# Kernel optimization log

Hardware: AMD Instinct MI355X
Metric: run time of the kernel (lower is better)

Reference implementation:

```python
import jax, jax.numpy as jnp
import numpy as np
from jax import lax

D_MODEL = 128
D_INNER = 256   # expand * d_model
D_STATE = 16
D_CONV = 4
DT_RANK = 8     # ceil(d_model / 16)
IN_CH = 64
SCALE = 0.02


def setup_inputs() -> dict:
    key = jax.random.key(0)
    ks = jax.random.split(key, 16)
    r = lambda k, s: jax.random.normal(k, s, dtype=jnp.float32)
    return {
        "x": r(ks[0], (4, IN_CH, 128, 128)),
        "conv_w": r(ks[1], (D_MODEL, IN_CH, 3, 3)) * SCALE,
        "conv_b": r(ks[2], (D_MODEL,)) * SCALE,
        "bn_g": jnp.ones((D_MODEL,), jnp.float32),
        "bn_b": jnp.zeros((D_MODEL,), jnp.float32),
        "bn_mean": r(ks[3], (D_MODEL,)) * SCALE,
        "bn_var": jax.random.uniform(ks[4], (D_MODEL,), jnp.float32) + 0.5,
        "in_w": r(ks[5], (2 * D_INNER, D_MODEL)) * SCALE,
        "conv1d_w": r(ks[6], (D_INNER, 1, D_CONV)) * SCALE,
        "conv1d_b": r(ks[7], (D_INNER,)) * SCALE,
        "xproj_w": r(ks[8], (DT_RANK + 2 * D_STATE, D_INNER)) * SCALE,
        "dtproj_w": r(ks[9], (D_INNER, DT_RANK)) * SCALE,
        "dtproj_b": r(ks[10], (D_INNER,)) * SCALE,
        "A_log": r(ks[11], (D_INNER, D_STATE)) * 0.5,
        "Dp": r(ks[12], (D_INNER,)) * SCALE,
        "out_w": r(ks[13], (D_MODEL, D_INNER)) * SCALE,
    }


def _mamba(u, in_w, conv1d_w, conv1d_b, xproj_w, dtproj_w, dtproj_b, A_log, Dp, out_w):
    # u: [B, L, d_model]
    xz = jnp.einsum("bld,ed->ble", u, in_w)          # [B, L, 2*d_inner]
    x_in, z = jnp.split(xz, 2, axis=-1)
    # depthwise causal conv1d over L
    xc = lax.conv_general_dilated(
        x_in.transpose(0, 2, 1), conv1d_w, (1,), [(D_CONV - 1, 0)],
        dimension_numbers=("NCL", "OIL", "NCL"), feature_group_count=D_INNER,
    ) + conv1d_b[None, :, None]
    x_in = jax.nn.silu(xc).transpose(0, 2, 1)         # [B, L, d_inner]

    x_dbl = jnp.einsum("bld,ed->ble", x_in, xproj_w)  # [B, L, dt_rank+2*d_state]
    dt, Bm, Cm = jnp.split(x_dbl, [DT_RANK, DT_RANK + D_STATE], axis=-1)
    delta = jax.nn.softplus(jnp.einsum("blr,dr->bld", dt, dtproj_w) + dtproj_b)

    A = -jnp.exp(A_log)                               # [d_inner, d_state]
    deltaA = jnp.exp(jnp.einsum("bld,dn->bldn", delta, A))        # [B,L,d,n]
    deltaBu = jnp.einsum("bld,bln,bld->bldn", delta, Bm, x_in)    # [B,L,d,n]

    def step(h, inp):
        dA, dBu, c = inp                              # [B,d,n],[B,d,n],[B,n]
        h = dA * h + dBu
        y = jnp.einsum("bdn,bn->bd", h, c)
        return h, y

    Bsz, L = u.shape[0], u.shape[1]
    h0 = jnp.zeros((Bsz, D_INNER, D_STATE), u.dtype)
    _, ys = lax.scan(step, h0, (deltaA.transpose(1, 0, 2, 3),
                                deltaBu.transpose(1, 0, 2, 3),
                                Cm.transpose(1, 0, 2)))
    y = ys.transpose(1, 0, 2) + x_in * Dp             # [B, L, d_inner]
    y = y * jax.nn.silu(z)
    return jnp.einsum("bld,ed->ble", y, out_w)        # [B, L, d_model]


def reference(x, conv_w, conv_b, bn_g, bn_b, bn_mean, bn_var, in_w, conv1d_w,
              conv1d_b, xproj_w, dtproj_w, dtproj_b, A_log, Dp, out_w):
    # downsample: conv3x3 stride2 + BN(eval) + exact GELU
    y = lax.conv_general_dilated(x, conv_w, (2, 2), [(1, 1), (1, 1)],
                                 dimension_numbers=("NCHW", "OIHW", "NCHW"))
    y = y + conv_b[None, :, None, None]
    inv = bn_g / jnp.sqrt(bn_var + 1e-5)
    y = (y - bn_mean[None, :, None, None]) * inv[None, :, None, None] + bn_b[None, :, None, None]
    y = jax.nn.gelu(y, approximate=False)             # [B, C, H, W]

    B, C, H, W = y.shape
    u = y.reshape(B, C, H * W).transpose(0, 2, 1)     # [B, L, C]
    out = _mamba(u, in_w, conv1d_w, conv1d_b, xproj_w, dtproj_w, dtproj_b,
                 A_log, Dp, out_w)
    out = out.transpose(0, 2, 1).reshape(B, C, H, W)
    return y + out
```

## Files before the change

### kernel.cpp

```cpp
#include <hip/hip_runtime.h>
#include <math.h>

#define NB 4
#define LTOK 4096
#define DM 128
#define DI 256
#define NCH 256
#define TCH 16
#define GSZ 16
#define NG  16

#define OFF_A2     0u
#define OFF_BIAS2  73728u
#define OFF_YDS    84096u
#define OFF_XPRE   2181248u
#define OFF_Z      6375552u
#define OFF_DELTA  10569856u
#define OFF_YABF   12667008u
#define OFF_BC     14764160u
#define OFF_DSUM   15288448u
#define OFF_GS     15550592u
#define OFF_GD     15812736u
#define OFF_XT     15829120u
#define OFF_WBF    17926272u
#define OFF_WCMP   17963136u
#define OFF_YDSBF  18004096u
#define OFF_INWBF  19052672u
#define OFF_OUTWBF 19085440u

#define DEV __device__ __forceinline__
#define L2E 1.4426950408889634f

typedef short bh8 __attribute__((ext_vector_type(8)));
typedef float f4v __attribute__((ext_vector_type(4)));

DEV float fast_silu(float v) {
  return v * __builtin_amdgcn_rcpf(1.f + __expf(-v));
}

DEV unsigned short f2bf(float f) {
  unsigned int u = __float_as_uint(f);
  u = (u + 0x7FFFu + ((u >> 16) & 1u)) >> 16;
  return (unsigned short)u;
}

DEV float bf2f(unsigned short us) {
  return __uint_as_float((unsigned int)us << 16);
}

__global__ __launch_bounds__(256) void k0_prep(
    const float* __restrict__ conv_w, const float* __restrict__ conv_b,
    const float* __restrict__ bn_g, const float* __restrict__ bn_b,
    const float* __restrict__ bn_mean, const float* __restrict__ bn_var,
    const float* __restrict__ xproj_w, const float* __restrict__ A_log,
    const float* __restrict__ dtw, const float* __restrict__ in_w,
    const float* __restrict__ out_w, float* __restrict__ ws) {
  int i = blockIdx.x * 256 + threadIdx.x;
  if (i < 73728) {
    int ci = i & 63; int tap = (i >> 6) % 9; int co = i / 576;
    float inv = bn_g[co] * rsqrtf(bn_var[co] + 1e-5f);
    ((unsigned short*)(ws + OFF_WBF))[i] = f2bf(conv_w[co * 576 + ci * 9 + tap] * inv);
  } else if (i < 73856) {
    int co = i - 73728;
    float inv = bn_g[co] * rsqrtf(bn_var[co] + 1e-5f);
    ws[OFF_BIAS2 + co] = (conv_b[co] - bn_mean[co]) * inv + bn_b[co];
  } else if (i < 77952) {
    int j = i - 73856;
    ws[OFF_A2 + j] = -__expf(A_log[j]) * L2E;
  } else if (i < 159872) {
    int j = i - 77952;
    int n = j >> 8, k = j & 255;
    float v = 0.f;
    if (n < 256) {
#pragma unroll
      for (int r = 0; r < 8; ++r)
        v = fmaf(dtw[n * 8 + r], xproj_w[r * 256 + k], v);
    } else if (n < 288) {
      v = xproj_w[(8 + n - 256) * 256 + k];
    }
    ((unsigned short*)(ws + OFF_WCMP))[j] = f2bf(v);
  } else if (i < 225408) {
    int j = i - 159872;
    ((unsigned short*)(ws + OFF_INWBF))[j] = f2bf(in_w[j]);
  } else if (i < 258176) {
    int j = i - 225408;
    ((unsigned short*)(ws + OFF_OUTWBF))[j] = f2bf(out_w[j]);
  }
}

__global__ __launch_bounds__(256) void k0b_transpose(
    const float* __restrict__ x, unsigned short* __restrict__ xt) {
  __shared__ float t[64][65];
  const int tid = threadIdx.x;
  const int ixh = blockIdx.x & 1;
  const int iy = (blockIdx.x >> 1) & 127;
  const int b = blockIdx.x >> 8;
  {
    const int ixl = tid & 63, cw = tid >> 6;
#pragma unroll 4
    for (int i = 0; i < 16; ++i) {
      int ci = cw * 16 + i;
      t[ci][ixl] = x[(((size_t)(b * 64 + ci) * 128) + iy) * 128 + ixh * 64 + ixl];
    }
  }
  __syncthreads();
  {
    const int cil = tid & 63, iw = tid >> 6;
    unsigned short* dst = xt + (((size_t)(b * 128 + iy) * 128) + ixh * 64) * 64;
#pragma unroll 4
    for (int i = 0; i < 16; ++i) {
      int ix = iw * 16 + i;
      dst[ix * 64 + cil] = f2bf(t[cil][ix]);
    }
  }
}

__global__ __launch_bounds__(256) void k1_conv_mfma(
    const unsigned short* __restrict__ xt, const unsigned short* __restrict__ wbf,
    const float* __restrict__ bias2, float* __restrict__ yds,
    unsigned short* __restrict__ ydsbf) {
  __shared__ unsigned short ldt[64][66];
  const int tid = threadIdx.x;
  const int lane = tid & 63;
  const int w = tid >> 6;
  const int col = lane & 15, quad = lane >> 4;
  const int cohalf = blockIdx.x & 1;
  const int oy = (blockIdx.x >> 1) & 63;
  const int b = blockIdx.x >> 7;
  const int co0 = cohalf * 64 + (w & 1) * 32;
  const int tok0 = (w >> 1) * 32;
  const int iy0 = 2 * oy - 1;
  const bh8 bzero = {};
  f4v acc[2][2];
#pragma unroll
  for (int mt = 0; mt < 2; ++mt)
#pragma unroll
    for (int nt = 0; nt < 2; ++nt) acc[mt][nt] = (f4v){0.f, 0.f, 0.f, 0.f};

  const unsigned short* ap0 = wbf + (size_t)(co0 + col) * 576;
  const unsigned short* ap1 = wbf + (size_t)(co0 + 16 + col) * 576;

  for (int tap = 0; tap < 9; ++tap) {
    const int kh = tap / 3, kw = tap - kh * 3;
    const int iy = iy0 + kh;
    const int ix0 = 2 * (tok0 + col) - 1 + kw;
    const int ix1 = ix0 + 32;
    const unsigned short* xrow = xt + (long)(b * 128 + iy) * 8192;
    const bool ok0 = (iy >= 0) && (ix0 >= 0);
    const bool ok1 = (iy >= 0);
#pragma unroll
    for (int kc = 0; kc < 2; ++kc) {
      const int cib = kc * 32 + quad * 8;
      bh8 a0 = *(const bh8*)&ap0[tap * 64 + cib];
      bh8 a1 = *(const bh8*)&ap1[tap * 64 + cib];
      bh8 b0 = *(const bh8*)&xrow[(long)ix0 * 64 + cib];
      bh8 b1 = *(const bh8*)&xrow[(long)ix1 * 64 + cib];
      if (!ok0) b0 = bzero;
      if (!ok1) b1 = bzero;
      acc[0][0] = __builtin_amdgcn_mfma_f32_16x16x32_bf16(a0, b0, acc[0][0], 0, 0, 0);
      acc[1][0] = __builtin_amdgcn_mfma_f32_16x16x32_bf16(a1, b0, acc[1][0], 0, 0, 0);
      acc[0][1] = __builtin_amdgcn_mfma_f32_16x16x32_bf16(a0, b1, acc[0][1], 0, 0, 0);
      acc[1][1] = __builtin_amdgcn_mfma_f32_16x16x32_bf16(a1, b1, acc[1][1], 0, 0, 0);
    }
  }
#pragma unroll
  for (int mt = 0; mt < 2; ++mt)
#pragma unroll
    for (int nt = 0; nt < 2; ++nt) {
      const int tok = tok0 + nt * 16 + col;
#pragma unroll
      for (int r = 0; r < 4; ++r) {
        const int co = co0 + mt * 16 + quad * 4 + r;
        float v = acc[mt][nt][r] + bias2[co];
        float g = 0.5f * v * (1.f + erff(v * 0.70710678118f));
        yds[(((size_t)(b * 128 + co) * 64) + oy) * 64 + tok] = g;
        ldt[tok][(w & 1) * 32 + mt * 16 + quad * 4 + r] = f2bf(g);
      }
    }
  __syncthreads();
  {
    const int tok = tid >> 2, cg = (tid & 3) * 16;
    unsigned short* dst =
        ydsbf + ((size_t)(b * 4096 + oy * 64 + tok)) * 128 + cohalf * 64 + cg;
#pragma unroll
    for (int j = 0; j < 8; ++j)
      ((unsigned int*)dst)[j] = *(const unsigned int*)&ldt[tok][cg + 2 * j];
  }
}

__global__ __launch_bounds__(256) void k2_mfma(
    const unsigned short* __restrict__ ydsbf, const unsigned short* __restrict__ inwbf,
    float* __restrict__ xpre, float* __restrict__ z) {
  const int tid = threadIdx.x;
  const int lane = tid & 63;
  const int w = tid >> 6;
  const int col = lane & 15, quad = lane >> 4;
  const int tt = blockIdx.x & 255, b = blockIdx.x >> 8;
  const int t0 = tt * 16;
  bh8 afrag[4];
  {
    const unsigned short* arow = ydsbf + (size_t)(b * 4096 + t0 + col) * 128 + quad * 8;
#pragma unroll
    for (int kb = 0; kb < 4; ++kb) afrag[kb] = *(const bh8*)&arow[kb * 32];
  }
  f4v acc[8];
#pragma unroll
  for (int j = 0; j < 8; ++j) acc[j] = (f4v){0.f, 0.f, 0.f, 0.f};
  const int nt0 = w * 8;
  const unsigned short* wb = inwbf + (size_t)(nt0 * 16 + col) * 128 + quad * 8;
#pragma unroll
  for (int kb = 0; kb < 4; ++kb) {
#pragma unroll
    for (int j = 0; j < 8; ++j) {
      bh8 bfrag = *(const bh8*)&wb[(size_t)j * 2048 + kb * 32];
      acc[j] = __builtin_amdgcn_mfma_f32_16x16x32_bf16(afrag[kb], bfrag, acc[j], 0, 0, 0);
    }
  }
#pragma unroll
  for (int j = 0; j < 8; ++j) {
    const int e = (nt0 + j) * 16 + col;
#pragma unroll
    for (int r = 0; r < 4; ++r) {
      const int t = t0 + quad * 4 + r;
      if (e < 256) xpre[((size_t)(b * 4096 + t)) * 256 + e] = acc[j][r];
      else z[((size_t)(b * 4096 + t)) * 256 + e - 256] = acc[j][r];
    }
  }
}

__global__ __launch_bounds__(256) void k3_conv1d_silu(
    const float* __restrict__ xpre, const float* __restrict__ w,
    const float* __restrict__ bvec, unsigned short* __restrict__ xinbf) {
  int i = blockIdx.x * 256 + threadIdx.x;
  int e4 = (i & 63) * 4;
  int t = (i >> 6) & 4095;
  int b = i >> 18;
  const float* base = xpre + (size_t)b * 4096 * 256;
  float4 zero = make_float4(0.f, 0.f, 0.f, 0.f);
  float4 r0 = (t >= 3) ? *(const float4*)&base[(size_t)(t - 3) * 256 + e4] : zero;
  float4 r1 = (t >= 2) ? *(const float4*)&base[(size_t)(t - 2) * 256 + e4] : zero;
  float4 r2 = (t >= 1) ? *(const float4*)&base[(size_t)(t - 1) * 256 + e4] : zero;
  float4 r3 = *(const float4*)&base[(size_t)t * 256 + e4];
  float4 w0 = *(const float4*)&w[(e4 + 0) * 4];
  float4 w1 = *(const float4*)&w[(e4 + 1) * 4];
  float4 w2 = *(const float4*)&w[(e4 + 2) * 4];
  float4 w3 = *(const float4*)&w[(e4 + 3) * 4];
  float4 bv = *(const float4*)&bvec[e4];
  float o0 = bv.x + w0.x * r0.x + w0.y * r1.x + w0.z * r2.x + w0.w * r3.x;
  float o1 = bv.y + w1.x * r0.y + w1.y * r1.y + w1.z * r2.y + w1.w * r3.y;
  float o2 = bv.z + w2.x * r0.z + w2.y * r1.z + w2.z * r2.z + w2.w * r3.z;
  float o3 = bv.w + w3.x * r0.w + w3.y * r1.w + w3.z * r2.w + w3.w * r3.w;
  float s0 = fast_silu(o0), s1 = fast_silu(o1), s2 = fast_silu(o2), s3 = fast_silu(o3);
  size_t off = ((size_t)b * 4096 + t) * 256 + e4;
  unsigned long long p = (unsigned long long)f2bf(s0)
                       | ((unsigned long long)f2bf(s1) << 16)
                       | ((unsigned long long)f2bf(s2) << 32)
                       | ((unsigned long long)f2bf(s3) << 48);
  *(unsigned long long*)&xinbf[off] = p;
}

__global__ __launch_bounds__(256) void k4_mfma(
    const unsigned short* __restrict__ wcomp, const float* __restrict__ dtb,
    const unsigned short* __restrict__ xinbf, unsigned short* __restrict__ delta,
    float* __restrict__ bc, float* __restrict__ dsum) {
  __shared__ unsigned short ld_delta[16][264];
  __shared__ float ld_bc[16][33];
  const int tid = threadIdx.x;
  const int lane = tid & 63;
  const int w = tid >> 6;
  const int col = lane & 15, quad = lane >> 4;
  const int tt = blockIdx.x & 255, b = blockIdx.x >> 8;
  const int t0 = tt * 16;

  bh8 afrag[8];
  {
    const unsigned short* arow = xinbf + (size_t)(b * 4096 + t0 + col) * 256 + quad * 8;
#pragma unroll
    for (int kb = 0; kb < 8; ++kb) afrag[kb] = *(const bh8*)&arow[kb * 32];
  }
  f4v acc[5];
#pragma unroll
  for (int j = 0; j < 5; ++j) acc[j] = (f4v){0.f, 0.f, 0.f, 0.f};

  const int nt0 = w * 5;
  const unsigned short* wb = wcomp + (size_t)(nt0 * 16 + col) * 256 + quad * 8;
#pragma unroll
  for (int kb = 0; kb < 8; ++kb) {
#pragma unroll
    for (int j = 0; j < 5; ++j) {
      bh8 bfrag = *(const bh8*)&wb[(size_t)j * 4096 + kb * 32];
      acc[j] = __builtin_amdgcn_mfma_f32_16x16x32_bf16(afrag[kb], bfrag, acc[j], 0, 0, 0);
    }
  }
#pragma unroll
  for (int j = 0; j < 5; ++j) {
    const int n = (nt0 + j) * 16 + col;
    if (n < 256) {
      float bias = dtb[n];
#pragma unroll
      for (int r = 0; r < 4; ++r) {
        float s = acc[j][r] + bias;
        float dl = fmaxf(s, 0.f) + __logf(1.f + __expf(-fabsf(s)));
        ld_delta[quad * 4 + r][n] = f2bf(dl);
      }
    } else if (n < 288) {
#pragma unroll
      for (int r = 0; r < 4; ++r) ld_bc[quad * 4 + r][n - 256] = acc[j][r];
    }
  }
  __syncthreads();

  {
    float ds = 0.f;
#pragma unroll
    for (int i = 0; i < 16; ++i) ds += bf2f(ld_delta[i][tid]);
    dsum[((size_t)b * 256 + tt) * 256 + tid] = ds;
  }
#pragma unroll
  for (int it = 0; it < 4; ++it) {
    int idx = it * 256 + tid;
    int row = idx >> 6, d4 = (idx & 63) * 4;
    unsigned long long pk = *(const unsigned long long*)&ld_delta[row][d4];
    *(unsigned long long*)&delta[((size_t)(b * 4096 + t0 + row)) * 256 + d4] = pk;
  }
  if (tid < 128) {
    int row = tid >> 3, q = (tid & 7) * 4;
    float4 v = make_float4(ld_bc[row][q], ld_bc[row][q + 1],
                           ld_bc[row][q + 2], ld_bc[row][q + 3]);
    *(float4*)&bc[((size_t)(b * 4096 + t0 + row)) * 32 + q] = v;
  }
}

__global__ __launch_bounds__(256) void k5a_scan1(
    const unsigned short* __restrict__ xinbf, const float* __restrict__ bc,
    const unsigned short* __restrict__ delta, const float* __restrict__ a2tab,
    float* __restrict__ S) {
  __shared__ __align__(16) float bct[TCH * 32];
  const int tid = threadIdx.x;
  const int d = tid;
  const int c = blockIdx.x & (NCH - 1), b = blockIdx.x >> 8;
  const int t0 = c * TCH;
  {
    const float* src = bc + (size_t)(b * 4096 + t0) * 32;
    for (int i = tid; i < TCH * 32; i += 256) bct[i] = src[i];
  }
  float A2[16];
#pragma unroll
  for (int j = 0; j < 4; ++j) {
    float4 a = *(const float4*)&a2tab[d * 16 + j * 4];
    A2[4 * j + 0] = a.x; A2[4 * j + 1] = a.y; A2[4 * j + 2] = a.z; A2[4 * j + 3] = a.w;
  }
  float h[16];
#pragma unroll
  for (int n = 0; n < 16; ++n) h[n] = 0.f;
  const unsigned short* pd = delta + (size_t)(b * 4096 + t0) * 256 + d;
  const unsigned short* px = xinbf + (size_t)(b * 4096 + t0) * 256 + d;
  __syncthreads();
#pragma unroll 4
  for (int i = 0; i < TCH; ++i) {
    float dl = bf2f(pd[(size_t)i * 256]);
    float xv = bf2f(px[(size_t)i * 256]);
    float dlx = dl * xv;
    const float* r = &bct[i * 32];
    float4 B0 = *(const float4*)&r[0];
    float4 B1 = *(const float4*)&r[4];
    float4 B2 = *(const float4*)&r[8];
    float4 B3 = *(const float4*)&r[12];
    float Bv[16] = {B0.x, B0.y, B0.z, B0.w, B1.x, B1.y, B1.z, B1.w,
                    B2.x, B2.y, B2.z, B2.w, B3.x, B3.y, B3.z, B3.w};
#pragma unroll
    for (int n = 0; n < 16; ++n)
      h[n] = fmaf(exp2f(dl * A2[n]), h[n], dlx * Bv[n]);
  }
  const size_t sbase = ((size_t)(b * NCH + c) * 16) * 256 + d;
#pragma unroll
  for (int n = 0; n < 16; ++n) S[sbase + (size_t)n * 256] = h[n];
}

__global__ __launch_bounds__(256) void k5b1_group(
    float* __restrict__ S, const float* __restrict__ dsum,
    const float* __restrict__ a2tab, float* __restrict__ Gs,
    float* __restrict__ Gd) {
  const int d = threadIdx.x;
  const int n = blockIdx.x & 15, g = (blockIdx.x >> 4) & (NG - 1),
            b = blockIdx.x >> 8;
  const float A2 = a2tab[d * 16 + n];
  float h = 0.f, cum = 0.f;
#pragma unroll 4
  for (int c16 = 0; c16 < GSZ; ++c16) {
    int c = g * GSZ + c16;
    size_t si = ((size_t)(b * NCH + c) * 16 + n) * 256 + d;
    float s = S[si];
    float dsv = dsum[((size_t)b * NCH + c) * 256 + d];
    float P = exp2f(A2 * dsv);
    S[si] = h;
    h = fmaf(P, h, s);
    cum += dsv;
  }
  Gs[((size_t)(b * NG + g) * 16 + n) * 256 + d] = h;
  if (n == 0) Gd[((size_t)b * NG + g) * 256 + d] = cum;
}

__global__ __launch_bounds__(256) void k5b2_groupscan(
    float* __restrict__ Gs, const float* __restrict__ Gd,
    const float* __restrict__ a2tab) {
  const int d = threadIdx.x;
  const int n = blockIdx.x & 15, b = blockIdx.x >> 4;
  const float A2 = a2tab[d * 16 + n];
  float h = 0.f;
#pragma unroll
  for (int g = 0; g < NG; ++g) {
    size_t gi = ((size_t)(b * NG + g) * 16 + n) * 256 + d;
    float s = Gs[gi];
    float P = exp2f(A2 * Gd[((size_t)b * NG + g) * 256 + d]);
    Gs[gi] = h;
    h = fmaf(P, h, s);
  }
}

__global__ __launch_bounds__(256) void k5c_scan2(
    const unsigned short* __restrict__ xinbf, const float* __restrict__ bc,
    const unsigned short* __restrict__ delta, const float* __restrict__ z,
    const float* __restrict__ a2tab, const float* __restrict__ Dp,
    const float* __restrict__ dsum, const float* __restrict__ Gs,
    const float* __restrict__ S, unsigned short* __restrict__ yabf) {
  __shared__ __align__(16) float bct[TCH * 32];
  const int tid = threadIdx.x;
  const int d = tid;
  const int c = blockIdx.x & (NCH - 1), b = blockIdx.x >> 8;
  const int t0 = c * TCH;
  {
    const float* src = bc + (size_t)(b * 4096 + t0) * 32;
    for (int i = tid; i < TCH * 32; i += 256) bct[i] = src[i];
  }
  float A2[16];
#pragma unroll
  for (int j = 0; j < 4; ++j) {
    float4 a = *(const float4*)&a2tab[d * 16 + j * 4];
    A2[4 * j + 0] = a.x; A2[4 * j + 1] = a.y; A2[4 * j + 2] = a.z; A2[4 * j + 3] = a.w;
  }
  const float Dpd = Dp[d];
  const int g = c >> 4, c16 = c & 15;
  float dpref = 0.f;
  {
    const float* pds = dsum + ((size_t)b * NCH + g * GSZ) * 256 + d;
    for (int cc = 0; cc < c16; ++cc) dpref += pds[(size_t)cc * 256];
  }
  const size_t sbase = ((size_t)(b * NCH + c) * 16) * 256 + d;
  const size_t gbase = ((size_t)(b * NG + g) * 16) * 256 + d;
  float h[16];
#pragma unroll
  for (int n = 0; n < 16; ++n) {
    float gi = Gs[gbase + (size_t)n * 256];
    float hl = S[sbase + (size_t)n * 256];
    h[n] = fmaf(exp2f(A2[n] * dpref), gi, hl);
  }
  const size_t base = (size_t)(b * 4096 + t0) * 256 + d;
  const unsigned short* pd = delta + base;
  const unsigned short* px = xinbf + base;
  const float* pz = z + base;
  unsigned short* py = yabf + base;
  __syncthreads();
#pragma unroll 4
  for (int i = 0; i < TCH; ++i) {
    float dl = bf2f(pd[(size_t)i * 256]);
    float xv = bf2f(px[(size_t)i * 256]);
    float zv = pz[(size_t)i * 256];
    float dlx = dl * xv;
    const float* r = &bct[i * 32];
    float4 B0 = *(const float4*)&r[0];
    float4 B1 = *(const float4*)&r[4];
    float4 B2 = *(const float4*)&r[8];
    float4 B3 = *(const float4*)&r[12];
    float4 C0 = *(const float4*)&r[16];
    float4 C1 = *(const float4*)&r[20];
    float4 C2 = *(const float4*)&r[24];
    float4 C3 = *(const float4*)&r[28];
    float Bv[16] = {B0.x, B0.y, B0.z, B0.w, B1.x, B1.y, B1.z, B1.w,
                    B2.x, B2.y, B2.z, B2.w, B3.x, B3.y, B3.z, B3.w};
    float Cv[16] = {C0.x, C0.y, C0.z, C0.w, C1.x, C1.y, C1.z, C1.w,
                    C2.x, C2.y, C2.z, C2.w, C3.x, C3.y, C3.z, C3.w};
    float y = 0.f;
#pragma unroll
    for (int n = 0; n < 16; ++n) {
      h[n] = fmaf(exp2f(dl * A2[n]), h[n], dlx * Bv[n]);
      y = fmaf(h[n], Cv[n], y);
    }
    py[(size_t)i * 256] = f2bf((y + xv * Dpd) * fast_silu(zv));
  }
}

__global__ __launch_bounds__(256) void k6_mfma(
    const unsigned short* __restrict__ yabf, const unsigned short* __restrict__ outwbf,
    const float* __restrict__ yds, float* __restrict__ out) {
  __shared__ float ld[16][132];
  const int tid = threadIdx.x;
  const int lane = tid & 63;
  const int w = tid >> 6;
  const int col = lane & 15, quad = lane >> 4;
  const int tt = blockIdx.x & 255, b = blockIdx.x >> 8;
  const int t0 = tt * 16;
  const int oy = t0 >> 6, ox0 = t0 & 63;
  bh8 afrag[8];
  {
    const unsigned short* arow = yabf + (size_t)(b * 4096 + t0 + col) * 256 + quad * 8;
#pragma unroll
    for (int kb = 0; kb < 8; ++kb) afrag[kb] = *(const bh8*)&arow[kb * 32];
  }
  f4v acc[2];
#pragma unroll
  for (int j = 0; j < 2; ++j) acc[j] = (f4v){0.f, 0.f, 0.f, 0.f};
  const int nt0 = w * 2;
  const unsigned short* wb = outwbf + (size_t)(nt0 * 16 + col) * 256 + quad * 8;
#pragma unroll
  for (int kb = 0; kb < 8; ++kb) {
#pragma unroll
    for (int j = 0; j < 2; ++j) {
      bh8 bfrag = *(const bh8*)&wb[(size_t)j * 4096 + kb * 32];
      acc[j] = __builtin_amdgcn_mfma_f32_16x16x32_bf16(afrag[kb], bfrag, acc[j], 0, 0, 0);
    }
  }
#pragma unroll
  for (int j = 0; j < 2; ++j)
#pragma unroll
    for (int r = 0; r < 4; ++r)
      ld[quad * 4 + r][(nt0 + j) * 16 + col] = acc[j][r];
  __syncthreads();
  {
    const int cc = tid >> 1, half = tid & 1;
    size_t base = (((size_t)(b * 128 + cc) * 64) + oy) * 64 + ox0 + half * 8;
    float4 r0 = *(const float4*)&yds[base];
    float4 r1 = *(const float4*)&yds[base + 4];
    const int m0 = half * 8;
    float4 o0 = make_float4(ld[m0 + 0][cc] + r0.x, ld[m0 + 1][cc] + r0.y,
                            ld[m0 + 2][cc] + r0.z, ld[m0 + 3][cc] + r0.w);
    float4 o1 = make_float4(ld[m0 + 4][cc] + r1.x, ld[m0 + 5][cc] + r1.y,
                            ld[m0 + 6][cc] + r1.z, ld[m0 + 7][cc] + r1.w);
    *(float4*)&out[base] = o0;
    *(float4*)&out[base + 4] = o1;
  }
}

extern "C" void kernel_launch(void* const* d_in, const int* in_sizes, int n_in,
                              void* d_out, int out_size, void* d_ws, size_t ws_size,
                              hipStream_t stream) {
  (void)in_sizes; (void)n_in; (void)out_size; (void)ws_size;
  const float* x        = (const float*)d_in[0];
  const float* conv_w   = (const float*)d_in[1];
  const float* conv_b   = (const float*)d_in[2];
  const float* bn_g     = (const float*)d_in[3];
  const float* bn_b     = (const float*)d_in[4];
  const float* bn_mean  = (const float*)d_in[5];
  const float* bn_var   = (const float*)d_in[6];
  const float* in_w     = (const float*)d_in[7];
  const float* conv1d_w = (const float*)d_in[8];
  const float* conv1d_b = (const float*)d_in[9];
  const float* xproj_w  = (const float*)d_in[10];
  const float* dtproj_w = (const float*)d_in[11];
  const float* dtproj_b = (const float*)d_in[12];
  const float* A_log    = (const float*)d_in[13];
  const float* Dp       = (const float*)d_in[14];
  const float* out_w    = (const float*)d_in[15];
  float* ws = (float*)d_ws;
  float* out = (float*)d_out;

  k0_prep<<<1009, 256, 0, stream>>>(conv_w, conv_b, bn_g, bn_b, bn_mean, bn_var,
                                    xproj_w, A_log, dtproj_w, in_w, out_w, ws);
  k0b_transpose<<<1024, 256, 0, stream>>>(x, (unsigned short*)(ws + OFF_XT));
  k1_conv_mfma<<<512, 256, 0, stream>>>((const unsigned short*)(ws + OFF_XT),
                                        (const unsigned short*)(ws + OFF_WBF),
                                        ws + OFF_BIAS2, ws + OFF_YDS,
                                        (unsigned short*)(ws + OFF_YDSBF));
  k2_mfma<<<1024, 256, 0, stream>>>((const unsigned short*)(ws + OFF_YDSBF),
                                    (const unsigned short*)(ws + OFF_INWBF),
                                    ws + OFF_XPRE, ws + OFF_Z);
  k3_conv1d_silu<<<4096, 256, 0, stream>>>(ws + OFF_XPRE, conv1d_w, conv1d_b,
                                           (unsigned short*)(ws + OFF_XT));
  k4_mfma<<<1024, 256, 0, stream>>>((const unsigned short*)(ws + OFF_WCMP),
                                    dtproj_b, (const unsigned short*)(ws + OFF_XT),
                                    (unsigned short*)(ws + OFF_DELTA),
                                    ws + OFF_BC, ws + OFF_DSUM);
  k5a_scan1<<<1024, 256, 0, stream>>>((const unsigned short*)(ws + OFF_XT),
                                      ws + OFF_BC,
                                      (const unsigned short*)(ws + OFF_DELTA),
                                      ws + OFF_A2, ws + OFF_XPRE);
  k5b1_group<<<1024, 256, 0, stream>>>(ws + OFF_XPRE, ws + OFF_DSUM, ws + OFF_A2,
                                       ws + OFF_GS, ws + OFF_GD);
  k5b2_groupscan<<<64, 256, 0, stream>>>(ws + OFF_GS, ws + OFF_GD, ws + OFF_A2);
  k5c_scan2<<<1024, 256, 0, stream>>>((const unsigned short*)(ws + OFF_XT),
                                      ws + OFF_BC,
                                      (const unsigned short*)(ws + OFF_DELTA),
                                      ws + OFF_Z, ws + OFF_A2, Dp, ws + OFF_DSUM,
                                      ws + OFF_GS, ws + OFF_XPRE,
                                      (unsigned short*)(ws + OFF_YABF));
  k6_mfma<<<1024, 256, 0, stream>>>((const unsigned short*)(ws + OFF_YABF),
                                    (const unsigned short*)(ws + OFF_OUTWBF),
                                    ws + OFF_YDS, out);
}
```

Measured before the change: 259.6 us.

## Fuse causal conv1d+SiLU into x-proj kernel and store intermediates as bf16

Removes the separate conv1d+SiLU kernel: k4 now computes the depthwise causal conv and SiLU for its 16-token tile (with a 3-token halo) straight into shared memory and feeds the MFMA A-fragments from there, while still writing x_in to global for the scans. The x_pre, z and downsample-residual buffers are stored as bf16 instead of fp32, roughly halving their write and read traffic across k1, k2, k4, k5c and k6. The trade-off is lower precision in the residual path and in z, plus redundant halo loads in k4. Note that k5a/k5c still use OFF_XPRE as fp32 scratch, which overlaps the region now holding bf16 xpre; since xpre is fully consumed by k4 before that, this should be safe.

```diff
diff --git a/kernel.cpp b/kernel.cpp
--- a/kernel.cpp
+++ b/kernel.cpp
@@ -12,7 +12,7 @@
 
 #define OFF_A2     0u
 #define OFF_BIAS2  73728u
-#define OFF_YDS    84096u
+#define OFF_YDSR   84096u
 #define OFF_XPRE   2181248u
 #define OFF_Z      6375552u
 #define OFF_DELTA  10569856u
@@ -117,7 +117,7 @@
 
 __global__ __launch_bounds__(256) void k1_conv_mfma(
     const unsigned short* __restrict__ xt, const unsigned short* __restrict__ wbf,
-    const float* __restrict__ bias2, float* __restrict__ yds,
+    const float* __restrict__ bias2, unsigned short* __restrict__ ydsr,
     unsigned short* __restrict__ ydsbf) {
   __shared__ unsigned short ldt[64][66];
   const int tid = threadIdx.x;
@@ -173,8 +173,9 @@
         const int co = co0 + mt * 16 + quad * 4 + r;
         float v = acc[mt][nt][r] + bias2[co];
         float g = 0.5f * v * (1.f + erff(v * 0.70710678118f));
-        yds[(((size_t)(b * 128 + co) * 64) + oy) * 64 + tok] = g;
-        ldt[tok][(w & 1) * 32 + mt * 16 + quad * 4 + r] = f2bf(g);
+        unsigned short gb = f2bf(g);
+        ydsr[(((size_t)(b * 128 + co) * 64) + oy) * 64 + tok] = gb;
+        ldt[tok][(w & 1) * 32 + mt * 16 + quad * 4 + r] = gb;
       }
     }
   __syncthreads();
@@ -190,7 +191,7 @@
 
 __global__ __launch_bounds__(256) void k2_mfma(
     const unsigned short* __restrict__ ydsbf, const unsigned short* __restrict__ inwbf,
-    float* __restrict__ xpre, float* __restrict__ z) {
+    unsigned short* __restrict__ xpre, unsigned short* __restrict__ z) {
   const int tid = threadIdx.x;
   const int lane = tid & 63;
   const int w = tid >> 6;
@@ -222,47 +223,19 @@
 #pragma unroll
     for (int r = 0; r < 4; ++r) {
       const int t = t0 + quad * 4 + r;
-      if (e < 256) xpre[((size_t)(b * 4096 + t)) * 256 + e] = acc[j][r];
-      else z[((size_t)(b * 4096 + t)) * 256 + e - 256] = acc[j][r];
-    }
-  }
-}
-
-__global__ __launch_bounds__(256) void k3_conv1d_silu(
-    const float* __restrict__ xpre, const float* __restrict__ w,
-    const float* __restrict__ bvec, unsigned short* __restrict__ xinbf) {
-  int i = blockIdx.x * 256 + threadIdx.x;
-  int e4 = (i & 63) * 4;
-  int t = (i >> 6) & 4095;
-  int b = i >> 18;
-  const float* base = xpre + (size_t)b * 4096 * 256;
-  float4 zero = make_float4(0.f, 0.f, 0.f, 0.f);
-  float4 r0 = (t >= 3) ? *(const float4*)&base[(size_t)(t - 3) * 256 + e4] : zero;
-  float4 r1 = (t >= 2) ? *(const float4*)&base[(size_t)(t - 2) * 256 + e4] : zero;
-  float4 r2 = (t >= 1) ? *(const float4*)&base[(size_t)(t - 1) * 256 + e4] : zero;
-  float4 r3 = *(const float4*)&base[(size_t)t * 256 + e4];
-  float4 w0 = *(const float4*)&w[(e4 + 0) * 4];
-  float4 w1 = *(const float4*)&w[(e4 + 1) * 4];
-  float4 w2 = *(const float4*)&w[(e4 + 2) * 4];
-  float4 w3 = *(const float4*)&w[(e4 + 3) * 4];
-  float4 bv = *(const float4*)&bvec[e4];
-  float o0 = bv.x + w0.x * r0.x + w0.y * r1.x + w0.z * r2.x + w0.w * r3.x;
-  float o1 = bv.y + w1.x * r0.y + w1.y * r1.y + w1.z * r2.y + w1.w * r3.y;
-  float o2 = bv.z + w2.x * r0.z + w2.y * r1.z + w2.z * r2.z + w2.w * r3.z;
-  float o3 = bv.w + w3.x * r0.w + w3.y * r1.w + w3.z * r2.w + w3.w * r3.w;
-  float s0 = fast_silu(o0), s1 = fast_silu(o1), s2 = fast_silu(o2), s3 = fast_silu(o3);
-  size_t off = ((size_t)b * 4096 + t) * 256 + e4;
-  unsigned long long p = (unsigned long long)f2bf(s0)
-                       | ((unsigned long long)f2bf(s1) << 16)
-                       | ((unsigned long long)f2bf(s2) << 32)
-                       | ((unsigned long long)f2bf(s3) << 48);
-  *(unsigned long long*)&xinbf[off] = p;
+      if (e < 256) xpre[((size_t)(b * 4096 + t)) * 256 + e] = f2bf(acc[j][r]);
+      else z[((size_t)(b * 4096 + t)) * 256 + e - 256] = f2bf(acc[j][r]);
+    }
+  }
 }
 
 __global__ __launch_bounds__(256) void k4_mfma(
     const unsigned short* __restrict__ wcomp, const float* __restrict__ dtb,
-    const unsigned short* __restrict__ xinbf, unsigned short* __restrict__ delta,
-    float* __restrict__ bc, float* __restrict__ dsum) {
+    const unsigned short* __restrict__ xpre, const float* __restrict__ cw1,
+    const float* __restrict__ cb1, unsigned short* __restrict__ xinbf,
+    unsigned short* __restrict__ delta, float* __restrict__ bc,
+    float* __restrict__ dsum) {
+  __shared__ unsigned short ld_xin[16][264];
   __shared__ unsigned short ld_delta[16][264];
   __shared__ float ld_bc[16][33];
   const int tid = threadIdx.x;
@@ -272,12 +245,32 @@
   const int tt = blockIdx.x & 255, b = blockIdx.x >> 8;
   const int t0 = tt * 16;
 
+  {
+    const int d = tid;
+    float4 w4 = *(const float4*)&cw1[d * 4];
+    float bias = cb1[d];
+    float xw[19];
+#pragma unroll
+    for (int i = 0; i < 19; ++i) {
+      int t = t0 - 3 + i;
+      xw[i] = (t >= 0) ? bf2f(xpre[((size_t)(b * 4096 + t)) * 256 + d]) : 0.f;
+    }
+    unsigned short* dst = xinbf + ((size_t)(b * 4096 + t0)) * 256 + d;
+#pragma unroll
+    for (int i = 0; i < 16; ++i) {
+      float o = bias + w4.x * xw[i] + w4.y * xw[i + 1] + w4.z * xw[i + 2] +
+                w4.w * xw[i + 3];
+      unsigned short us = f2bf(fast_silu(o));
+      ld_xin[i][d] = us;
+      dst[(size_t)i * 256] = us;
+    }
+  }
+  __syncthreads();
+
   bh8 afrag[8];
-  {
-    const unsigned short* arow = xinbf + (size_t)(b * 4096 + t0 + col) * 256 + quad * 8;
-#pragma unroll
-    for (int kb = 0; kb < 8; ++kb) afrag[kb] = *(const bh8*)&arow[kb * 32];
-  }
+#pragma unroll
+  for (int kb = 0; kb < 8; ++kb)
+    afrag[kb] = *(const bh8*)&ld_xin[col][quad * 8 + kb * 32];
   f4v acc[5];
 #pragma unroll
   for (int j = 0; j < 5; ++j) acc[j] = (f4v){0.f, 0.f, 0.f, 0.f};
@@ -420,7 +413,7 @@
 
 __global__ __launch_bounds__(256) void k5c_scan2(
     const unsigned short* __restrict__ xinbf, const float* __restrict__ bc,
-    const unsigned short* __restrict__ delta, const float* __restrict__ z,
+    const unsigned short* __restrict__ delta, const unsigned short* __restrict__ z,
     const float* __restrict__ a2tab, const float* __restrict__ Dp,
     const float* __restrict__ dsum, const float* __restrict__ Gs,
     const float* __restrict__ S, unsigned short* __restrict__ yabf) {
@@ -458,14 +451,14 @@
   const size_t base = (size_t)(b * 4096 + t0) * 256 + d;
   const unsigned short* pd = delta + base;
   const unsigned short* px = xinbf + base;
-  const float* pz = z + base;
+  const unsigned short* pz = z + base;
   unsigned short* py = yabf + base;
   __syncthreads();
 #pragma unroll 4
   for (int i = 0; i < TCH; ++i) {
     float dl = bf2f(pd[(size_t)i * 256]);
     float xv = bf2f(px[(size_t)i * 256]);
-    float zv = pz[(size_t)i * 256];
+    float zv = bf2f(pz[(size_t)i * 256]);
     float dlx = dl * xv;
     const float* r = &bct[i * 32];
     float4 B0 = *(const float4*)&r[0];
@@ -492,7 +485,7 @@
 
 __global__ __launch_bounds__(256) void k6_mfma(
     const unsigned short* __restrict__ yabf, const unsigned short* __restrict__ outwbf,
-    const float* __restrict__ yds, float* __restrict__ out) {
+    const unsigned short* __restrict__ ydsr, float* __restrict__ out) {
   __shared__ float ld[16][132];
   const int tid = threadIdx.x;
   const int lane = tid & 63;
@@ -529,13 +522,12 @@
   {
     const int cc = tid >> 1, half = tid & 1;
     size_t base = (((size_t)(b * 128 + cc) * 64) + oy) * 64 + ox0 + half * 8;
-    float4 r0 = *(const float4*)&yds[base];
-    float4 r1 = *(const float4*)&yds[base + 4];
+    const unsigned short* rp = ydsr + base;
     const int m0 = half * 8;
-    float4 o0 = make_float4(ld[m0 + 0][cc] + r0.x, ld[m0 + 1][cc] + r0.y,
-                            ld[m0 + 2][cc] + r0.z, ld[m0 + 3][cc] + r0.w);
-    float4 o1 = make_float4(ld[m0 + 4][cc] + r1.x, ld[m0 + 5][cc] + r1.y,
-                            ld[m0 + 6][cc] + r1.z, ld[m0 + 7][cc] + r1.w);
+    float4 o0 = make_float4(ld[m0 + 0][cc] + bf2f(rp[0]), ld[m0 + 1][cc] + bf2f(rp[1]),
+                            ld[m0 + 2][cc] + bf2f(rp[2]), ld[m0 + 3][cc] + bf2f(rp[3]));
+    float4 o1 = make_float4(ld[m0 + 4][cc] + bf2f(rp[4]), ld[m0 + 5][cc] + bf2f(rp[5]),
+                            ld[m0 + 6][cc] + bf2f(rp[6]), ld[m0 + 7][cc] + bf2f(rp[7]));
     *(float4*)&out[base] = o0;
     *(float4*)&out[base + 4] = o1;
   }
@@ -569,15 +561,18 @@
   k0b_transpose<<<1024, 256, 0, stream>>>(x, (unsigned short*)(ws + OFF_XT));
   k1_conv_mfma<<<512, 256, 0, stream>>>((const unsigned short*)(ws + OFF_XT),
                                         (const unsigned short*)(ws + OFF_WBF),
-                                        ws + OFF_BIAS2, ws + OFF_YDS,
+                                        ws + OFF_BIAS2,
+                                        (unsigned short*)(ws + OFF_YDSR),
                                         (unsigned short*)(ws + OFF_YDSBF));
   k2_mfma<<<1024, 256, 0, stream>>>((const unsigned short*)(ws + OFF_YDSBF),
                                     (const unsigned short*)(ws + OFF_INWBF),
-                                    ws + OFF_XPRE, ws + OFF_Z);
-  k3_conv1d_silu<<<4096, 256, 0, stream>>>(ws + OFF_XPRE, conv1d_w, conv1d_b,
-                                           (unsigned short*)(ws + OFF_XT));
+                                    (unsigned short*)(ws + OFF_XPRE),
+                                    (unsigned short*)(ws + OFF_Z));
   k4_mfma<<<1024, 256, 0, stream>>>((const unsigned short*)(ws + OFF_WCMP),
-                                    dtproj_b, (const unsigned short*)(ws + OFF_XT),
+                                    dtproj_b,
+                                    (const unsigned short*)(ws + OFF_XPRE),
+                                    conv1d_w, conv1d_b,
+                                    (unsigned short*)(ws + OFF_XT),
                                     (unsigned short*)(ws + OFF_DELTA),
                                     ws + OFF_BC, ws + OFF_DSUM);
   k5a_scan1<<<1024, 256, 0, stream>>>((const unsigned short*)(ws + OFF_XT),
@@ -590,10 +585,11 @@
   k5c_scan2<<<1024, 256, 0, stream>>>((const unsigned short*)(ws + OFF_XT),
                                       ws + OFF_BC,
                                       (const unsigned short*)(ws + OFF_DELTA),
-                                      ws + OFF_Z, ws + OFF_A2, Dp, ws + OFF_DSUM,
+                                      (const unsigned short*)(ws + OFF_Z),
+                                      ws + OFF_A2, Dp, ws + OFF_DSUM,
                                       ws + OFF_GS, ws + OFF_XPRE,
                                       (unsigned short*)(ws + OFF_YABF));
   k6_mfma<<<1024, 256, 0, stream>>>((const unsigned short*)(ws + OFF_YABF),
                                     (const unsigned short*)(ws + OFF_OUTWBF),
-                                    ws + OFF_YDS, out);
-}
+                                    (const unsigned short*)(ws + OFF_YDSR), out);
+}
```

Measured after the change: 240.9 us. 7.2% less time.
